# Optimization experiments

Measured on AMD Instinct MI355X. Metric: run time of the kernel, lower is better.

## Reference

```python
import jax, jax.numpy as jnp
import numpy as np

T, B, V, F = 30, 32, 32, 128   # len_pred, batch, n_vehicles, feature_size
L, LF = 256, 64                # n_lanes, lane_feature_size
H = 8                          # n_heads
DH = F // H                    # head dim
HIST = 10                      # leading mask dim reduced by any()


def setup_inputs() -> dict:
    key = jax.random.key(0)
    ks = jax.random.split(key, 16)
    s = 0.05
    return {
        "vehicles":    jax.random.normal(ks[0], (T, B, V, F), jnp.float32),
        "initial_pos": jax.random.normal(ks[1], (T, B, V, F), jnp.float32),
        "lanes":       jax.random.normal(ks[2], (B, L, LF), jnp.float32),
        "mask_lanes":  jax.random.randint(ks[3], (HIST, B, L), 0, 2).astype(bool),
        # key_lanes / value_lanes: Linear(LF -> F)
        "Wk": jax.random.normal(ks[4], (F, LF), jnp.float32) * s,
        "bk": jax.random.normal(ks[5], (F,), jnp.float32) * s,
        "Wv": jax.random.normal(ks[6], (F, LF), jnp.float32) * s,
        "bv": jax.random.normal(ks[7], (F,), jnp.float32) * s,
        # query / relation_lanes: Conv2d(F, F, (1,1)) == pointwise Linear(F -> F)
        "Wq": jax.random.normal(ks[8], (F, F), jnp.float32) * s,
        "bq": jax.random.normal(ks[9], (F,), jnp.float32) * s,
        "Wr": jax.random.normal(ks[10], (F, F), jnp.float32) * s,
        "br": jax.random.normal(ks[11], (F,), jnp.float32) * s,
        # attention_combine: Linear(F -> F)
        "Wc": jax.random.normal(ks[12], (F, F), jnp.float32) * s,
        "bc": jax.random.normal(ks[13], (F,), jnp.float32) * s,
    }


def reference(vehicles, initial_pos, lanes, mask_lanes,
              Wk, bk, Wv, bv, Wq, bq, Wr, br, Wc, bc):
    v = vehicles + initial_pos                                   # [T,B,V,F]
    # lane projections -> [B,H,L,DH]
    k = (lanes @ Wk.T + bk).reshape(B, L, H, DH).transpose(0, 2, 1, 3)
    val = (lanes @ Wv.T + bv).reshape(B, L, H, DH).transpose(0, 2, 1, 3)
    # vehicle projections (1x1 conv == linear over feature dim) -> [T,B,H,V,DH]
    q = (v @ Wq.T + bq).reshape(T, B, V, H, DH).transpose(0, 1, 3, 2, 4)
    r = (v @ Wr.T + br).reshape(T, B, V, H, DH).transpose(0, 1, 3, 2, 4)
    # mask: any over leading dims -> [B,L]
    mask = jnp.any(mask_lanes, axis=0)
    scores = jnp.einsum('tbhvd,bhld->tbhvl', q, k) / jnp.sqrt(jnp.float32(DH))
    scores = jnp.where(mask[None, :, None, None, :], scores, jnp.float32(-1e9))
    p = jax.nn.softmax(scores, axis=-1)                          # [T,B,H,V,L]
    att = jnp.exp(jnp.einsum('tbhvl,bhld->tbhvd', p, jax.nn.log_sigmoid(val)))
    # faithful to original: raw reshape [T,B,H,V,DH] -> [T,B,V,F] (no permute back)
    out = (r * att).reshape(T, B, V, F)
    return out @ Wc.T + bc + v - 2.0 * initial_pos
```

## Files before the change

### kernel.cpp

```cpp
#include <hip/hip_runtime.h>
#include <hip/hip_bf16.h>
#include <math.h>

#define T_ 30
#define B_ 32
#define V_ 32
#define F_ 128
#define L_ 256
#define LF_ 64
#define H_ 8
#define DH_ 16
#define HIST_ 10

typedef __attribute__((ext_vector_type(4))) float floatx4;
typedef __attribute__((ext_vector_type(8))) short shortx8;
typedef __attribute__((ext_vector_type(4))) unsigned short ushortx4;

#define MFMA_BF16(a, b, c) __builtin_amdgcn_mfma_f32_16x16x32_bf16(a, b, c, 0, 0, 0)

__device__ inline unsigned short f2bf_rne(float x) {
    unsigned int u = __builtin_bit_cast(unsigned int, x);
    unsigned int r = (u + 0x7fffu + ((u >> 16) & 1u)) >> 16;
    return (unsigned short)r;
}
__device__ inline unsigned short f2bf_trunc(float x) {
    return (unsigned short)(__builtin_bit_cast(unsigned int, x) >> 16);
}
__device__ inline float bf2f(unsigned short u) {
    return __builtin_bit_cast(float, (unsigned int)u << 16);
}
__device__ inline ushortx4 cvt4(floatx4 a) {
    ushortx4 r;
    r.x = f2bf_rne(a.x); r.y = f2bf_rne(a.y);
    r.z = f2bf_rne(a.z); r.w = f2bf_rne(a.w);
    return r;
}

__global__ __launch_bounds__(256, 2) void k_proj(
    const float* __restrict__ lanes, const int* __restrict__ mask,
    const float* __restrict__ veh, const float* __restrict__ ip,
    const float* __restrict__ Wk, const float* __restrict__ bk,
    const float* __restrict__ Wv, const float* __restrict__ bv,
    const float* __restrict__ Wq, const float* __restrict__ bq,
    const float* __restrict__ Wr, const float* __restrict__ br,
    unsigned short* __restrict__ kproj, unsigned short* __restrict__ lsvT,
    float* __restrict__ maskb, unsigned short* __restrict__ qb,
    unsigned short* __restrict__ rb, unsigned short* __restrict__ resid) {
    __shared__ unsigned short smem[32768];
    __shared__ float mloc[64];
    int tid = threadIdx.x;

    if (blockIdx.x < 128) {
        unsigned short* WkF = smem;
        unsigned short* WvF = smem + 8192;
        int m0 = blockIdx.x * 64;
        int b = m0 >> 8;
        if (tid < 64) {
            int row = m0 + tid;
            int any = 0;
#pragma unroll
            for (int hh = 0; hh < HIST_; ++hh) any |= mask[hh * (B_ * L_) + row];
            float fm = any ? 1.0f : 0.0f;
            maskb[row] = fm;
            mloc[tid] = fm;
        }
        for (int g = tid; g < 1024; g += 256) {
            int frag = g >> 6, l = g & 63, cc = l & 15, qq = l >> 4;
            int nt = frag >> 1, ks = frag & 1;
            int n = nt * 16 + cc, k0 = ks * 32 + qq * 8;
            floatx4 a0 = *(const floatx4*)(Wk + n * LF_ + k0);
            floatx4 a1 = *(const floatx4*)(Wk + n * LF_ + k0 + 4);
            *(ushortx4*)(WkF + g * 8) = cvt4(a0);
            *(ushortx4*)(WkF + g * 8 + 4) = cvt4(a1);
            floatx4 b0 = *(const floatx4*)(Wv + n * LF_ + k0);
            floatx4 b1 = *(const floatx4*)(Wv + n * LF_ + k0 + 4);
            *(ushortx4*)(WvF + g * 8) = cvt4(b0);
            *(ushortx4*)(WvF + g * 8 + 4) = cvt4(b1);
        }
        __syncthreads();
        int lane = tid & 63, w = tid >> 6;
        int c = lane & 15, quad = lane >> 4;
        int mw = m0 + w * 16;
        shortx8 aF[2];
#pragma unroll
        for (int ks = 0; ks < 2; ++ks) {
            const float* xp = lanes + (size_t)(mw + c) * LF_ + ks * 32 + quad * 8;
            floatx4 x0 = *(const floatx4*)(xp);
            floatx4 x1 = *(const floatx4*)(xp + 4);
            ushortx4 lo = cvt4(x0), hi = cvt4(x1);
            shortx8 af;
            af[0]=(short)lo.x; af[1]=(short)lo.y; af[2]=(short)lo.z; af[3]=(short)lo.w;
            af[4]=(short)hi.x; af[5]=(short)hi.y; af[6]=(short)hi.z; af[7]=(short)hi.w;
            aF[ks] = af;
        }
        floatx4 mk = *(const floatx4*)(mloc + w * 16 + quad * 4);
        int lbase = (mw & 255) + quad * 4;
#pragma unroll
        for (int nt = 0; nt < 8; ++nt) {
            floatx4 acck = {0.f, 0.f, 0.f, 0.f}, accv = {0.f, 0.f, 0.f, 0.f};
#pragma unroll
            for (int ks = 0; ks < 2; ++ks) {
                shortx8 bkf = *(const shortx8*)(WkF + ((nt * 2 + ks) * 64 + lane) * 8);
                shortx8 bvf = *(const shortx8*)(WvF + ((nt * 2 + ks) * 64 + lane) * 8);
                acck = MFMA_BF16(aF[ks], bkf, acck);
                accv = MFMA_BF16(aF[ks], bvf, accv);
            }
            int n = nt * 16 + c;
            float bkn = bk[n], bvn = bv[n];
            ushortx4 vout;
#pragma unroll
            for (int reg = 0; reg < 4; ++reg) {
                size_t row = mw + quad * 4 + reg;
                kproj[row * F_ + n] = f2bf_rne(acck[reg] + bkn);
                float xv = accv[reg] + bvn;
                float ls = fminf(xv, 0.f) - log1pf(__expf(-fabsf(xv)));
                vout[reg] = (mk[reg] > 0.5f) ? f2bf_rne(ls) : (unsigned short)0;
            }
            *(ushortx4*)(lsvT + ((size_t)b * F_ + n) * L_ + lbase) = vout;
        }
    } else {
        unsigned short* WqF = smem;
        unsigned short* WrF = smem + 16384;
        for (int g = tid; g < 2048; g += 256) {
            int frag = g >> 6, l = g & 63, cc = l & 15, qq = l >> 4;
            int nt = frag >> 2, ks = frag & 3;
            int n = nt * 16 + cc, k0 = ks * 32 + qq * 8;
            floatx4 a0 = *(const floatx4*)(Wq + n * F_ + k0);
            floatx4 a1 = *(const floatx4*)(Wq + n * F_ + k0 + 4);
            *(ushortx4*)(WqF + g * 8) = cvt4(a0);
            *(ushortx4*)(WqF + g * 8 + 4) = cvt4(a1);
            floatx4 b0 = *(const floatx4*)(Wr + n * F_ + k0);
            floatx4 b1 = *(const floatx4*)(Wr + n * F_ + k0 + 4);
            *(ushortx4*)(WrF + g * 8) = cvt4(b0);
            *(ushortx4*)(WrF + g * 8 + 4) = cvt4(b1);
        }
        __syncthreads();
        int lane = tid & 63, w = tid >> 6;
        int c = lane & 15, quad = lane >> 4;
        int m0 = (blockIdx.x - 128) * 64 + w * 16;
        shortx8 aF[4];
#pragma unroll
        for (int ks = 0; ks < 4; ++ks) {
            size_t off = (size_t)(m0 + c) * F_ + ks * 32 + quad * 8;
            floatx4 v0 = *(const floatx4*)(veh + off);
            floatx4 v1 = *(const floatx4*)(veh + off + 4);
            floatx4 i0 = *(const floatx4*)(ip + off);
            floatx4 i1 = *(const floatx4*)(ip + off + 4);
            ushortx4 lo = cvt4(v0 + i0), hi = cvt4(v1 + i1);
            shortx8 af;
            af[0]=(short)lo.x; af[1]=(short)lo.y; af[2]=(short)lo.z; af[3]=(short)lo.w;
            af[4]=(short)hi.x; af[5]=(short)hi.y; af[6]=(short)hi.z; af[7]=(short)hi.w;
            aF[ks] = af;
            *(ushortx4*)(resid + off) = cvt4(v0 - i0);
            *(ushortx4*)(resid + off + 4) = cvt4(v1 - i1);
        }
        const float QSCALE = 0.25f * 1.4426950408889634f;
#pragma unroll
        for (int nt = 0; nt < 8; ++nt) {
            floatx4 accq = {0.f, 0.f, 0.f, 0.f}, accr = {0.f, 0.f, 0.f, 0.f};
#pragma unroll
            for (int ks = 0; ks < 4; ++ks) {
                shortx8 bqf = *(const shortx8*)(WqF + ((nt * 4 + ks) * 64 + lane) * 8);
                shortx8 brf = *(const shortx8*)(WrF + ((nt * 4 + ks) * 64 + lane) * 8);
                accq = MFMA_BF16(aF[ks], bqf, accq);
                accr = MFMA_BF16(aF[ks], brf, accr);
            }
            int n = nt * 16 + c;
            float bqn = bq[n], brn = br[n];
#pragma unroll
            for (int reg = 0; reg < 4; ++reg) {
                size_t row = m0 + quad * 4 + reg;
                qb[row * F_ + n] = f2bf_rne((accq[reg] + bqn) * QSCALE);
                rb[row * F_ + n] = f2bf_rne(accr[reg] + brn);
            }
        }
    }
}

__global__ __launch_bounds__(256, 2) void k_attn(
    const unsigned short* __restrict__ kproj, const unsigned short* __restrict__ lsvT,
    const float* __restrict__ maskb, const unsigned short* __restrict__ qbuf,
    const unsigned short* __restrict__ rbuf, unsigned short* __restrict__ ratt) {
    __shared__ unsigned short kS[256 * 24];
    __shared__ unsigned short vT[16 * 264];
    __shared__ unsigned short pE[4 * 4096];

    int tid = threadIdx.x;
    int bh = blockIdx.x & 255;
    int tc = blockIdx.x >> 8;
    int h = bh & 7;
    int b = bh >> 3;

    const unsigned short* kbase = kproj + ((size_t)b * L_) * F_ + h * DH_;
#pragma unroll
    for (int it = 0; it < 2; ++it) {
        int id = it * 256 + tid;
        int l = id >> 1, half = id & 1;
        shortx8 kv = *(const shortx8*)(kbase + (size_t)l * F_ + half * 8);
        *(shortx8*)(kS + l * 24 + half * 8) = kv;
    }
    {
        int d = tid >> 4, c16 = tid & 15;
        const unsigned short* vrow = lsvT + ((size_t)b * F_ + h * DH_ + d) * L_ + c16 * 16;
        shortx8 v0 = *(const shortx8*)(vrow);
        shortx8 v1 = *(const shortx8*)(vrow + 8);
        *(shortx8*)(vT + d * 264 + c16 * 16) = v0;
        *(shortx8*)(vT + d * 264 + c16 * 16 + 8) = v1;
    }
    __syncthreads();

    int lane = tid & 63, w = tid >> 6;
    int c = lane & 15, quad = lane >> 4;

    shortx8 kF[16];
#pragma unroll
    for (int lt = 0; lt < 16; ++lt) {
        shortx8 z = {0, 0, 0, 0, 0, 0, 0, 0};
        kF[lt] = (quad < 2) ? *(const shortx8*)(kS + (lt * 16 + c) * 24 + quad * 8) : z;
    }
    shortx8 vF[8];
#pragma unroll
    for (int kk = 0; kk < 8; ++kk)
        vF[kk] = *(const shortx8*)(vT + c * 264 + kk * 32 + quad * 8);
    shortx8 mF[8];
#pragma unroll
    for (int kk = 0; kk < 8; ++kk) {
        const float* mp = maskb + b * L_ + kk * 32 + quad * 8;
        floatx4 ma = *(const floatx4*)(mp);
        floatx4 mb2 = *(const floatx4*)(mp + 4);
        shortx8 mf;
        mf[0]=(short)f2bf_trunc(ma.x); mf[1]=(short)f2bf_trunc(ma.y);
        mf[2]=(short)f2bf_trunc(ma.z); mf[3]=(short)f2bf_trunc(ma.w);
        mf[4]=(short)f2bf_trunc(mb2.x); mf[5]=(short)f2bf_trunc(mb2.y);
        mf[6]=(short)f2bf_trunc(mb2.z); mf[7]=(short)f2bf_trunc(mb2.w);
        mF[kk] = mf;
    }

    unsigned short* pEw = pE + w * 4096;
    int wr_c = c * 8 + (quad & 1) * 4;
    int wr_q = (quad >> 1) * 128;
    floatx4 z4 = {0.f, 0.f, 0.f, 0.f};

    for (int mtl = w; mtl < 15; mtl += 4) {
        int mt = tc * 15 + mtl;
        int q0 = mt << 4;
        int t = q0 >> 5, v0 = q0 & 31;
        size_t qrow0 = ((size_t)(t * B_ + b) * V_ + v0 + c) * F_ + h * DH_;

        shortx8 qF = {0, 0, 0, 0, 0, 0, 0, 0};
        if (quad < 2) qF = *(const shortx8*)(qbuf + qrow0 + quad * 8);

#pragma unroll
        for (int lt = 0; lt < 16; ++lt) {
            floatx4 s = MFMA_BF16(kF[lt], qF, z4);
            ushortx4 ep;
#pragma unroll
            for (int reg = 0; reg < 4; ++reg)
                ep[reg] = f2bf_trunc(__builtin_amdgcn_exp2f(s[reg]));
            *(ushortx4*)(pEw + (lt >> 1) * 512 + (lt & 1) * 256 + wr_q + wr_c) = ep;
        }

        floatx4 cU = z4, cN = z4;
#pragma unroll
        for (int kk = 0; kk < 8; ++kk) {
            shortx8 bP = *(const shortx8*)(pEw + (kk * 64 + lane) * 8);
            cU = MFMA_BF16(vF[kk], bP, cU);
            cN = MFMA_BF16(mF[kk], bP, cN);
        }
        float inv2 = __builtin_amdgcn_rcpf(cN[0]) * 1.4426950408889634f;
        ushortx4 rv = *(const ushortx4*)(rbuf + qrow0 + quad * 4);
        ushortx4 ob;
#pragma unroll
        for (int reg = 0; reg < 4; ++reg) {
            float att = __builtin_amdgcn_exp2f(cU[reg] * inv2);
            ob[reg] = f2bf_rne(bf2f(rv[reg]) * att);
        }
        *(ushortx4*)(ratt + (((size_t)t * B_ + b) * H_ + h) * (V_ * DH_)
                    + (v0 + c) * DH_ + quad * 4) = ob;
    }
}

__global__ __launch_bounds__(256, 2) void k_out(
    const unsigned short* __restrict__ ratt, const float* __restrict__ Wc,
    const float* __restrict__ bc, const unsigned short* __restrict__ resid,
    float* __restrict__ out) {
    __shared__ unsigned short WcF[16384];
    int tid = threadIdx.x;
    for (int g = tid; g < 2048; g += 256) {
        int frag = g >> 6, l = g & 63, cc = l & 15, qq = l >> 4;
        int nt = frag >> 2, ks = frag & 3;
        int n = nt * 16 + cc, k0 = ks * 32 + qq * 8;
        floatx4 a0 = *(const floatx4*)(Wc + n * F_ + k0);
        floatx4 a1 = *(const floatx4*)(Wc + n * F_ + k0 + 4);
        *(ushortx4*)(WcF + g * 8) = cvt4(a0);
        *(ushortx4*)(WcF + g * 8 + 4) = cvt4(a1);
    }
    __syncthreads();
    int lane = tid & 63, w = tid >> 6;
    int c = lane & 15, quad = lane >> 4;
    int m0 = blockIdx.x * 64 + w * 16;
    shortx8 aF[4];
#pragma unroll
    for (int ks = 0; ks < 4; ++ks)
        aF[ks] = *(const shortx8*)(ratt + (size_t)(m0 + c) * F_ + ks * 32 + quad * 8);
#pragma unroll
    for (int np = 0; np < 4; ++np) {
        int nt0 = np * 2, nt1 = np * 2 + 1;
        floatx4 acc0 = {0.f, 0.f, 0.f, 0.f}, acc1 = {0.f, 0.f, 0.f, 0.f};
#pragma unroll
        for (int ks = 0; ks < 4; ++ks) {
            shortx8 b0 = *(const shortx8*)(WcF + ((nt0 * 4 + ks) * 64 + lane) * 8);
            shortx8 b1 = *(const shortx8*)(WcF + ((nt1 * 4 + ks) * 64 + lane) * 8);
            acc0 = MFMA_BF16(aF[ks], b0, acc0);
            acc1 = MFMA_BF16(aF[ks], b1, acc1);
        }
        int n0 = nt0 * 16 + c, n1 = nt1 * 16 + c;
        float bc0 = bc[n0], bc1 = bc[n1];
#pragma unroll
        for (int reg = 0; reg < 4; ++reg) {
            size_t row = m0 + quad * 4 + reg;
            size_t o0 = row * F_ + n0, o1 = row * F_ + n1;
            out[o0] = acc0[reg] + bc0 + bf2f(resid[o0]);
            out[o1] = acc1[reg] + bc1 + bf2f(resid[o1]);
        }
    }
}

extern "C" void kernel_launch(void* const* d_in, const int* in_sizes, int n_in,
                              void* d_out, int out_size, void* d_ws, size_t ws_size,
                              hipStream_t stream) {
    const float* vehicles    = (const float*)d_in[0];
    const float* initial_pos = (const float*)d_in[1];
    const float* lanes       = (const float*)d_in[2];
    const int*   mask        = (const int*)d_in[3];
    const float* Wk = (const float*)d_in[4];
    const float* bk = (const float*)d_in[5];
    const float* Wv = (const float*)d_in[6];
    const float* bv = (const float*)d_in[7];
    const float* Wq = (const float*)d_in[8];
    const float* bq = (const float*)d_in[9];
    const float* Wr = (const float*)d_in[10];
    const float* br = (const float*)d_in[11];
    const float* Wc = (const float*)d_in[12];
    const float* bc = (const float*)d_in[13];
    float* out = (float*)d_out;

    char* p = (char*)d_ws;
    float* maskb = (float*)p;                   p += ((B_ * L_ * 4 + 255) / 256) * 256;
    unsigned short* kproj = (unsigned short*)p; p += ((size_t)B_ * L_ * F_ * 2 + 255) / 256 * 256;
    unsigned short* lsvT  = (unsigned short*)p; p += ((size_t)B_ * F_ * L_ * 2 + 255) / 256 * 256;
    unsigned short* qb    = (unsigned short*)p; p += ((size_t)T_ * B_ * V_ * F_ * 2 + 255) / 256 * 256;
    unsigned short* rb    = (unsigned short*)p; p += ((size_t)T_ * B_ * V_ * F_ * 2 + 255) / 256 * 256;
    unsigned short* rattb = (unsigned short*)p; p += ((size_t)T_ * B_ * V_ * F_ * 2 + 255) / 256 * 256;
    unsigned short* resid = (unsigned short*)p; p += ((size_t)T_ * B_ * V_ * F_ * 2 + 255) / 256 * 256;

    k_proj<<<128 + (T_ * B_ * V_) / 64, 256, 0, stream>>>(
        lanes, mask, vehicles, initial_pos, Wk, bk, Wv, bv, Wq, bq, Wr, br,
        kproj, lsvT, maskb, qb, rb, resid);
    k_attn<<<4 * B_ * H_, 256, 0, stream>>>(kproj, lsvT, maskb, qb, rb, rattb);
    k_out<<<(T_ * B_ * V_) / 64, 256, 0, stream>>>(rattb, Wc, bc, resid, out);
}
```

Baseline: 148.1 us.

## Store q/r head-major and give each attention block twice as many tiles

The projection kernel now writes the scaled query and the relation projections in a head-major layout [b,h,t,v,d] instead of row-major [t,b,v,f]. Each attention tile can then read its q and r values from one contiguous stretch instead of strided rows. The attention grid is halved so each block processes 30 query tiles rather than 15. This spreads the per-block cost of staging K, V and the mask over more work. The trade-off is fewer blocks in flight, which may hurt latency hiding. The projection kernel's scattered 2-byte stores also get a different address pattern.

After: 143.0 us. 3.5% less time.

```diff
diff --git a/kernel.cpp b/kernel.cpp
--- a/kernel.cpp
+++ b/kernel.cpp
@@ -44,8 +44,8 @@
     const float* __restrict__ Wq, const float* __restrict__ bq,
     const float* __restrict__ Wr, const float* __restrict__ br,
     unsigned short* __restrict__ kproj, unsigned short* __restrict__ lsvT,
-    float* __restrict__ maskb, unsigned short* __restrict__ qb,
-    unsigned short* __restrict__ rb, unsigned short* __restrict__ resid) {
+    float* __restrict__ maskb, unsigned short* __restrict__ qhm,
+    unsigned short* __restrict__ rhm, unsigned short* __restrict__ resid) {
     __shared__ unsigned short smem[32768];
     __shared__ float mloc[64];
     int tid = threadIdx.x;
@@ -169,9 +169,12 @@
             float bqn = bq[n], brn = br[n];
 #pragma unroll
             for (int reg = 0; reg < 4; ++reg) {
-                size_t row = m0 + quad * 4 + reg;
-                qb[row * F_ + n] = f2bf_rne((accq[reg] + bqn) * QSCALE);
-                rb[row * F_ + n] = f2bf_rne(accr[reg] + brn);
+                int row = m0 + quad * 4 + reg;
+                int t = row >> 10, rem = row & 1023;
+                int b = rem >> 5, v = rem & 31;
+                size_t hidx = ((size_t)((b * 8 + nt) * 30 + t) << 9) + (v << 4) + c;
+                qhm[hidx] = f2bf_rne((accq[reg] + bqn) * QSCALE);
+                rhm[hidx] = f2bf_rne(accr[reg] + brn);
             }
         }
     }
@@ -179,8 +182,8 @@
 
 __global__ __launch_bounds__(256, 2) void k_attn(
     const unsigned short* __restrict__ kproj, const unsigned short* __restrict__ lsvT,
-    const float* __restrict__ maskb, const unsigned short* __restrict__ qbuf,
-    const unsigned short* __restrict__ rbuf, unsigned short* __restrict__ ratt) {
+    const float* __restrict__ maskb, const unsigned short* __restrict__ qhm,
+    const unsigned short* __restrict__ rhm, unsigned short* __restrict__ ratt) {
     __shared__ unsigned short kS[256 * 24];
     __shared__ unsigned short vT[16 * 264];
     __shared__ unsigned short pE[4 * 4096];
@@ -236,19 +239,21 @@
         mF[kk] = mf;
     }
 
+    const unsigned short* qhead = qhm + ((size_t)(b * 8 + h) * 30) * 512;
+    const unsigned short* rhead = rhm + ((size_t)(b * 8 + h) * 30) * 512;
+
     unsigned short* pEw = pE + w * 4096;
     int wr_c = c * 8 + (quad & 1) * 4;
     int wr_q = (quad >> 1) * 128;
     floatx4 z4 = {0.f, 0.f, 0.f, 0.f};
 
-    for (int mtl = w; mtl < 15; mtl += 4) {
-        int mt = tc * 15 + mtl;
-        int q0 = mt << 4;
-        int t = q0 >> 5, v0 = q0 & 31;
-        size_t qrow0 = ((size_t)(t * B_ + b) * V_ + v0 + c) * F_ + h * DH_;
+    for (int mtl = w; mtl < 30; mtl += 4) {
+        int mt = tc * 30 + mtl;
+        int t = mt >> 1, v0 = (mt & 1) * 16;
+        size_t qtile = (size_t)t * 512 + v0 * 16;
 
         shortx8 qF = {0, 0, 0, 0, 0, 0, 0, 0};
-        if (quad < 2) qF = *(const shortx8*)(qbuf + qrow0 + quad * 8);
+        if (quad < 2) qF = *(const shortx8*)(qhead + qtile + c * 16 + quad * 8);
 
 #pragma unroll
         for (int lt = 0; lt < 16; ++lt) {
@@ -268,7 +273,7 @@
             cN = MFMA_BF16(mF[kk], bP, cN);
         }
         float inv2 = __builtin_amdgcn_rcpf(cN[0]) * 1.4426950408889634f;
-        ushortx4 rv = *(const ushortx4*)(rbuf + qrow0 + quad * 4);
+        ushortx4 rv = *(const ushortx4*)(rhead + qtile + c * 16 + quad * 4);
         ushortx4 ob;
 #pragma unroll
         for (int reg = 0; reg < 4; ++reg) {
@@ -349,14 +354,14 @@
     float* maskb = (float*)p;                   p += ((B_ * L_ * 4 + 255) / 256) * 256;
     unsigned short* kproj = (unsigned short*)p; p += ((size_t)B_ * L_ * F_ * 2 + 255) / 256 * 256;
     unsigned short* lsvT  = (unsigned short*)p; p += ((size_t)B_ * F_ * L_ * 2 + 255) / 256 * 256;
-    unsigned short* qb    = (unsigned short*)p; p += ((size_t)T_ * B_ * V_ * F_ * 2 + 255) / 256 * 256;
-    unsigned short* rb    = (unsigned short*)p; p += ((size_t)T_ * B_ * V_ * F_ * 2 + 255) / 256 * 256;
+    unsigned short* qhm   = (unsigned short*)p; p += ((size_t)T_ * B_ * V_ * F_ * 2 + 255) / 256 * 256;
+    unsigned short* rhm   = (unsigned short*)p; p += ((size_t)T_ * B_ * V_ * F_ * 2 + 255) / 256 * 256;
     unsigned short* rattb = (unsigned short*)p; p += ((size_t)T_ * B_ * V_ * F_ * 2 + 255) / 256 * 256;
     unsigned short* resid = (unsigned short*)p; p += ((size_t)T_ * B_ * V_ * F_ * 2 + 255) / 256 * 256;
 
     k_proj<<<128 + (T_ * B_ * V_) / 64, 256, 0, stream>>>(
         lanes, mask, vehicles, initial_pos, Wk, bk, Wv, bv, Wq, bq, Wr, br,
-        kproj, lsvT, maskb, qb, rb, resid);
-    k_attn<<<4 * B_ * H_, 256, 0, stream>>>(kproj, lsvT, maskb, qb, rb, rattb);
+        kproj, lsvT, maskb, qhm, rhm, resid);
+    k_attn<<<2 * B_ * H_, 256, 0, stream>>>(kproj, lsvT, maskb, qhm, rhm, rattb);
     k_out<<<(T_ * B_ * V_) / 64, 256, 0, stream>>>(rattb, Wc, bc, resid, out);
 }
```
